# Optimization experiments

Hardware: AMD Instinct MI355X
Metric: run time of the kernel (lower is better)

The kernel has to match this reference:

```python
import jax, jax.numpy as jnp
import numpy as np

T, B, L, S = 2048, 64, 32, 256
NEG = -1e30  # effective -inf, safe under logaddexp


def setup_inputs() -> dict:
    key = jax.random.key(0)
    k1, k2, k3 = jax.random.split(key, 3)
    inputs = jax.random.normal(k1, (T, B, L), dtype=jnp.float32)
    targets = jax.random.randint(k2, (B, S), 0, L)
    input_lengths = jnp.full((B,), T, dtype=jnp.int32)
    target_lengths = jnp.full((B,), S, dtype=jnp.int32)
    # learned transition matrix (param of ASGLoss); small random for a non-trivial test
    transition = 0.1 * jax.random.normal(k3, (L, L), dtype=jnp.float32)
    return {"transition": transition, "inputs": inputs, "targets": targets,
            "input_lengths": input_lengths, "target_lengths": target_lengths}


def _fcc_scores(transition, inputs, input_lengths):
    # Fully-connected forward: alpha_t[i] = emit_t[i] + logsumexp_j(alpha_{t-1}[j] + trans[i,j])
    alpha0 = inputs[0]  # [B, L]

    def step(alpha, emit):
        new = emit + jax.nn.logsumexp(alpha[:, None, :] + transition[None, :, :], axis=2)
        return new, new

    _, rest = jax.lax.scan(step, alpha0, inputs[1:])
    alphas = jnp.concatenate([alpha0[None], rest], axis=0)  # [T, B, L]
    b = jnp.arange(inputs.shape[1])
    # causal DP: alpha at t = len-1 is exactly the score for that length
    return jax.nn.logsumexp(alphas[input_lengths - 1, b], axis=-1)  # [B]


def _fac_scores(transition, inputs, targets, input_lengths, target_lengths):
    # Force-aligned forward over target positions s:
    # alpha_t[s] = emit_t[tgt_s] + logaddexp(alpha_{t-1}[s] + trans[tgt_s,tgt_s],
    #                                        alpha_{t-1}[s-1] + trans[tgt_s,tgt_{s-1}])
    Tn, Bn, _ = inputs.shape
    Sn = targets.shape[1]
    # gathered emissions for target labels: [T, B, S]
    emit = jnp.take_along_axis(inputs, jnp.broadcast_to(targets[None], (Tn, Bn, Sn)), axis=2)
    self_tr = transition[targets, targets]                       # [B, S] stay score
    prev = jnp.concatenate([targets[:, :1], targets[:, :-1]], 1)
    move_tr = transition[targets, prev]                          # [B, S] move score (s=0 unused)

    alpha0 = jnp.where((jnp.arange(Sn) == 0)[None, :], emit[0], NEG)  # only s=0 at t=0

    def step(alpha, e):
        stay = alpha + self_tr
        moved = jnp.concatenate(
            [jnp.full_like(alpha[:, :1], NEG), alpha[:, :-1] + move_tr[:, 1:]], axis=1)
        new = e + jnp.logaddexp(stay, moved)
        return new, new

    _, rest = jax.lax.scan(step, alpha0, emit[1:])
    alphas = jnp.concatenate([alpha0[None], rest], axis=0)  # [T, B, S]
    b = jnp.arange(Bn)
    return alphas[input_lengths - 1, b, target_lengths - 1]  # [B]


def reference(transition, inputs, targets, input_lengths, target_lengths):
    # original clamps targets to input length; S <= T here so it's a no-op
    fcc = _fcc_scores(transition, inputs, input_lengths)
    fac = _fac_scores(transition, inputs, targets, input_lengths, target_lengths)
    result = fcc - fac  # [B]
    return result.mean()  # reduction='mean'
```

## Files before the change

kernel.cpp:

```cpp
#include <hip/hip_runtime.h>
#include <math.h>

static constexpr int TB = 64;
static constexpr int LL = 32;
static constexpr int SS = 256;
static constexpr int STRIDE_T = TB * LL;

static constexpr int NCH = 16;
static constexpr int NI  = NCH - 2;
static constexpr int NSCAN = 2 + 2 * NI;

static constexpr int OF_FCC  = 0;
static constexpr int OF_FACF = 992;
static constexpr int OF_FACB = 1312;
static constexpr int WSB     = 1632;
static constexpr int OF_DIFF = TB * WSB;

#define LN2F 0.69314718055994530942f
#define NEGF (-1e30f)
#define SBAR() __builtin_amdgcn_sched_barrier(0)

#define BARX() { asm volatile("s_waitcnt lgkmcnt(0)" ::: "memory"); \
                 __builtin_amdgcn_s_barrier(); \
                 asm volatile("" ::: "memory"); }

template<int CTL>
__device__ __forceinline__ float dpp_f(float x, float oldv) {
  return __int_as_float(__builtin_amdgcn_update_dpp(
      __float_as_int(oldv), __float_as_int(x), CTL, 0xF, 0xF, false));
}
template<int M>
__device__ __forceinline__ int rot_i(int x) {
  return __builtin_amdgcn_update_dpp(0, x, 0x120 + M, 0xF, 0xF, false);
}

typedef unsigned uint2v __attribute__((ext_vector_type(2)));
__device__ __forceinline__ float xsum16(float x) {
  uint2v r = __builtin_amdgcn_permlane16_swap(__float_as_uint(x), __float_as_uint(x), false, false);
  return __uint_as_float(r.x) + __uint_as_float(r.y);
}
__device__ __forceinline__ float xsum32(float x) {
  uint2v r = __builtin_amdgcn_permlane32_swap(__float_as_uint(x), __float_as_uint(x), false, false);
  return __uint_as_float(r.x) + __uint_as_float(r.y);
}
__device__ __forceinline__ float bperm(int addr, float src) {
  return __int_as_float(__builtin_amdgcn_ds_bpermute(addr, __float_as_int(src)));
}

template<int M>
struct Calib {
  __device__ static __forceinline__ void run(const float* trans, int lam, int i, float* Ec) {
    Ec[M] = __expf(trans[i * LL + rot_i<M>(lam)]);
    Calib<M + 1>::run(trans, lam, i, Ec);
  }
};
template<> struct Calib<16> {
  __device__ static __forceinline__ void run(const float*, int, int, float*) {}
};
template<int M>
struct CalibT {
  __device__ static __forceinline__ void run(const float* trans, int lam, int i, float* Ec) {
    Ec[M] = __expf(trans[rot_i<M>(lam) * LL + i]);
    CalibT<M + 1>::run(trans, lam, i, Ec);
  }
};
template<> struct CalibT<16> {
  __device__ static __forceinline__ void run(const float*, int, int, float*) {}
};

#define ROT_MUL(DST, SRC, COEF, ROT) \
  asm("v_mul_f32_dpp %0, %1, %2 row_ror:" #ROT " row_mask:0xf bank_mask:0xf" \
      : "=v"(DST) : "v"(SRC), "v"(COEF))
#define ROT_FMAC(ACC, SRC, COEF, ROT) \
  asm("v_fmac_f32_dpp %0, %1, %2 row_ror:" #ROT " row_mask:0xf bank_mask:0xf" \
      : "+v"(ACC) : "v"(SRC), "v"(COEF))

#define STEP16(EC) { \
  float a0 = EC[0] * A, a1, a2, a3, a4, a5, a6, a7; \
  ROT_MUL(a1, A, EC[1], 1); ROT_MUL(a2, A, EC[2], 2); ROT_MUL(a3, A, EC[3], 3); \
  ROT_MUL(a4, A, EC[4], 4); ROT_MUL(a5, A, EC[5], 5); ROT_MUL(a6, A, EC[6], 6); \
  ROT_MUL(a7, A, EC[7], 7); \
  ROT_FMAC(a0, A, EC[8], 8);   ROT_FMAC(a1, A, EC[9], 9); \
  ROT_FMAC(a2, A, EC[10], 10); ROT_FMAC(a3, A, EC[11], 11); \
  ROT_FMAC(a4, A, EC[12], 12); ROT_FMAC(a5, A, EC[13], 13); \
  ROT_FMAC(a6, A, EC[14], 14); ROT_FMAC(a7, A, EC[15], 15); \
  part = ((a0 + a1) + (a2 + a3)) + ((a4 + a5) + (a6 + a7)); }


#define FCC_RENORM() { \
  unsigned uu = (unsigned)__builtin_amdgcn_readfirstlane((int)__float_as_uint(A)); \
  int ex = (int)((uu >> 23) & 255) - 127; \
  A = ldexpf(A, -ex); Kt += ex; }

#define LDBLK(R, TBASE) { \
  _Pragma("unroll") for (int k = 0; k < 4; ++k) { \
    int tt = (TBASE) + 2 * k + rowoff; tt = tt > lenm1 ? lenm1 : tt; \
    R[k] = gpl[(size_t)tt * STRIDE_T]; } \
  SBAR(); }
#define LDBLKD(R, TBASE) { \
  _Pragma("unroll") for (int k = 0; k < 4; ++k) { \
    int tt = (TBASE) + 2 * k + rowoff; \
    tt = tt < 0 ? 0 : (tt > lenm1 ? lenm1 : tt); \
    R[k] = gpl[(size_t)tt * STRIDE_T]; } \
  SBAR(); }

#define FCC_BLOCK8(R) { \
  float eb[8]; \
  _Pragma("unroll") for (int k = 0; k < 4; ++k) { \
    float e_ = __expf(R[k]); \
    eb[2 * k]     = bperm(adE, e_); \
    eb[2 * k + 1] = bperm(adO, e_); } \
  { float part; STEP16(Ec1); A = eb[0] * xsum16(part); } \
  { float part; STEP16(Ec2); A = eb[1] * xsum32(part); } \
  { float part; STEP16(Ec1); A = eb[2] * xsum16(part); } \
  { float part; STEP16(Ec2); A = eb[3] * xsum32(part); } \
  { float part; STEP16(Ec1); A = eb[4] * xsum16(part); } \
  { float part; STEP16(Ec2); A = eb[5] * xsum32(part); } \
  { float part; STEP16(Ec1); A = eb[6] * xsum16(part); } \
  { float part; STEP16(Ec2); A = eb[7] * xsum32(part); } \
  FCC_RENORM(); }

#define FCC_BWDBLK8(R) { \
  float eb[8]; \
  _Pragma("unroll") for (int k = 0; k < 4; ++k) { \
    float e_ = __expf(R[k]); \
    eb[2 * k]     = bperm(adE, e_); \
    eb[2 * k + 1] = bperm(adO, e_); } \
  { A *= eb[7]; float part; STEP16(E1T); A = xsum16(part); } \
  { A *= eb[6]; float part; STEP16(E2T); A = xsum32(part); } \
  { A *= eb[5]; float part; STEP16(E1T); A = xsum16(part); } \
  { A *= eb[4]; float part; STEP16(E2T); A = xsum32(part); } \
  { A *= eb[3]; float part; STEP16(E1T); A = xsum16(part); } \
  { A *= eb[2]; float part; STEP16(E2T); A = xsum32(part); } \
  { A *= eb[1]; float part; STEP16(E1T); A = xsum16(part); } \
  { A *= eb[0]; float part; STEP16(E2T); A = xsum32(part); } \
  FCC_RENORM(); }


#define FAC_BOUNDARY_S() { \
  float maxA = fmaxf(fmaxf(A0, A1), fmaxf(A2, A3)); \
  if (maxA > 0.f) { \
    int ex = (int)((__float_as_uint(maxA) >> 23) & 255) - 127; \
    A0 = ldexpf(A0, -ex); A1 = ldexpf(A1, -ex); \
    A2 = ldexpf(A2, -ex); A3 = ldexpf(A3, -ex); \
    m += (float)ex; \
  } \
  float mp = dpp_f<0x138>(m, NEGF); m = (m == NEGF) ? mp : m; \
  mp = dpp_f<0x138>(m, NEGF);       m = (m == NEGF) ? mp : m; \
  mp = dpp_f<0x138>(m, NEGF); \
  float dlt = fminf(mp - m, 50.0f); \
  Sin = exp2f(dlt); }

#define FSTEPE(R) { \
  float c0 = Er[R].x * ST[0], c1 = Er[R].y * ST[1]; \
  float c2 = Er[R].z * ST[2], c3 = Er[R].w * ST[3]; \
  float v0 = Er[R].x * CM[0], v1 = Er[R].y * CM[1]; \
  float v2 = Er[R].z * CM[2], v3 = Er[R].w * CM[3]; \
  float ap = dpp_f<0x138>(A3, 0.f);  \
  float n0 = fmaf(v0 * Sin, ap, c0 * A0); \
  float n1 = fmaf(v1, A0, c1 * A1); \
  float n2 = fmaf(v2, A1, c2 * A2); \
  float n3 = fmaf(v3, A2, c3 * A3); \
  A0 = n0; A1 = n1; A2 = n2; A3 = n3; }

#define FRD16(PB, BASE) { \
  _Pragma("unroll") for (int r = 0; r < 16; ++r) Er[r] = sFE[PB][(BASE) + r][l]; }

#define FSTE8A() { FSTEPE(0); FSTEPE(1); FSTEPE(2); FSTEPE(3); \
                   FSTEPE(4); FSTEPE(5); FSTEPE(6); FSTEPE(7); }
#define FSTE8B() { FSTEPE(8); FSTEPE(9); FSTEPE(10); FSTEPE(11); \
                   FSTEPE(12); FSTEPE(13); FSTEPE(14); FSTEPE(15); }

#define FACF_CON32(PB) { \
  float4 Er[16]; \
  FRD16(PB, 0); \
  FSTE8A(); FAC_BOUNDARY_S(); \
  FSTE8B(); FAC_BOUNDARY_S(); \
  FRD16(PB, 16); \
  FSTE8A(); FAC_BOUNDARY_S(); \
  FSTE8B(); FAC_BOUNDARY_S(); }

#define FACF_TAIL32(PB, CNT) { \
  float4 Er[16]; \
  FRD16(PB, 0); \
  _Pragma("unroll") for (int r = 0; r < 16; ++r) { \
    if (r >= (CNT)) break; \
    FSTEPE(r); \
    if (r == 7) { FAC_BOUNDARY_S(); } } \
  if ((CNT) > 16) { \
    FAC_BOUNDARY_S(); \
    FRD16(PB, 16); \
    _Pragma("unroll") for (int r = 0; r < 16; ++r) { \
      if (r + 16 >= (CNT)) break; \
      FSTEPE(r); \
      if (r == 7) { FAC_BOUNDARY_S(); } } } }

#define FACB_BOUNDARY_S() { \
  float maxA = fmaxf(fmaxf(A0, A1), fmaxf(A2, A3)); \
  if (maxA > 0.f) { \
    int ex = (int)((__float_as_uint(maxA) >> 23) & 255) - 127; \
    A0 = ldexpf(A0, -ex); A1 = ldexpf(A1, -ex); \
    A2 = ldexpf(A2, -ex); A3 = ldexpf(A3, -ex); \
    m += (float)ex; \
  } \
  float mp = dpp_f<0x130>(m, NEGF); m = (m == NEGF) ? mp : m; \
  mp = dpp_f<0x130>(m, NEGF);       m = (m == NEGF) ? mp : m; \
  mp = dpp_f<0x130>(m, NEGF); \
  float dlt = fminf(mp - m, 50.0f); \
  Sb = exp2f(dlt); }

#define FBSTEPE(R) { \
  float c0 = Er[R].x * ST[0], c1 = Er[R].y * ST[1]; \
  float c2 = Er[R].z * ST[2], c3 = Er[R].w * ST[3]; \
  float w0 = Er[R].y * CM[0], w1 = Er[R].z * CM[1], w2 = Er[R].w * CM[2]; \
  float en3 = dpp_f<0x130>(Er[R].x, 0.f);  \
  float w3 = en3 * CM[3]; \
  float an = dpp_f<0x130>(A0, 0.f); \
  float n0 = fmaf(w0, A1, c0 * A0); \
  float n1 = fmaf(w1, A2, c1 * A1); \
  float n2 = fmaf(w2, A3, c2 * A2); \
  float n3 = fmaf(w3 * Sb, an, c3 * A3); \
  A0 = n0; A1 = n1; A2 = n2; A3 = n3; }

#define FBST8D() { FBSTEPE(15); FBSTEPE(14); FBSTEPE(13); FBSTEPE(12); \
                   FBSTEPE(11); FBSTEPE(10); FBSTEPE(9);  FBSTEPE(8); }
#define FBST8L() { FBSTEPE(7);  FBSTEPE(6);  FBSTEPE(5);  FBSTEPE(4); \
                   FBSTEPE(3);  FBSTEPE(2);  FBSTEPE(1);  FBSTEPE(0); }

#define FACB_CON32(PB) { \
  float4 Er[16]; \
  FRD16(PB, 16); \
  FBST8D(); FACB_BOUNDARY_S(); \
  FBST8L(); FACB_BOUNDARY_S(); \
  FRD16(PB, 0); \
  FBST8D(); FACB_BOUNDARY_S(); \
  FBST8L(); FACB_BOUNDARY_S(); }


#define FHLD32(Q, K) ({ \
  int tt_ = (isfwd ? (1 + 32 * (Q)) : (lenm1 - 32 * (Q) - 31)) + 2 * (K) + rowoff; \
  tt_ = tt_ < 0 ? 0 : (tt_ > lenm1 ? lenm1 : tt_); \
  gpl[(size_t)tt_ * STRIDE_T]; })

#define PRODE(PB, KK, RV) { \
  float e_ = __expf(RV); \
  float4 E0_, E1_; \
  E0_.x = bperm(adA[0], e_); E0_.y = bperm(adA[1], e_); \
  E0_.z = bperm(adA[2], e_); E0_.w = bperm(adA[3], e_); \
  E1_.x = bperm(adB[0], e_); E1_.y = bperm(adB[1], e_); \
  E1_.z = bperm(adB[2], e_); E1_.w = bperm(adB[3], e_); \
  sFE[PB][2 * (KK)][l]     = E0_; \
  sFE[PB][2 * (KK) + 1][l] = E1_; }


extern "C" __global__ __launch_bounds__(192, 1)
void asg_main(const float* __restrict__ trans, const float* __restrict__ inputs,
              const int* __restrict__ targets, const int* __restrict__ ilen,
              const int* __restrict__ tlen, float* __restrict__ ws) {
  const int tid = (int)threadIdx.x;
  const int w = tid >> 6;
  const int l = tid & 63;
  const int lam1 = l & 31;
  const int lam2 = (l & 15) | ((l >> 5) << 4);
  const int rowoff = l >> 5;
  const int bid = (int)blockIdx.x;

  __shared__ float4 sFE[2][32][64];

  if (bid < 2 * TB) {
    const int role = bid >> 6;
    const int b    = bid & 63;
    const int len = ilen[b];
    const int lenm1 = len - 1;
    const int Lsteps = lenm1;
    const int nbf = (Lsteps / 2) & ~31;
    const int nff = Lsteps - nbf;
    const bool isfwd = (role == 0);
    const int nsteps = isfwd ? nff : nbf;
    const int nph = (nsteps + 31) >> 5;
    const float* gpl = inputs + (size_t)b * LL + lam1;
    float* P = ws + (size_t)b * WSB;

    if (w == 0) {
      __builtin_amdgcn_s_setprio(1);
      int tg[4];
      #pragma unroll
      for (int q = 0; q < 4; ++q) tg[q] = targets[b * SS + 4 * l + q];
      float ST[4], CM[4];
      #pragma unroll
      for (int q = 0; q < 4; ++q) ST[q] = __expf(trans[tg[q] * LL + tg[q]]);

      if (isfwd) {
        CM[0] = (l == 0) ? 0.f : __expf(trans[tg[0] * LL + targets[b * SS + 4 * l - 1]]);
        #pragma unroll
        for (int q = 1; q < 4; ++q) CM[q] = __expf(trans[tg[q] * LL + tg[q - 1]]);

        float A0 = (l == 0) ? __expf(inputs[(size_t)b * LL + tg[0]]) : 0.f;
        float A1 = 0.f, A2 = 0.f, A3 = 0.f;
        float m  = (l == 0) ? 0.f : NEGF;
        float Sin;
        FAC_BOUNDARY_S();
        for (int p = 0; p < nph; p += 2) {
          BARX();
          { const int rem = nsteps - 32 * p;
            if (rem >= 32) { FACF_CON32(0); } else { FACF_TAIL32(0, rem); } }
          BARX();
          if (p + 1 < nph) {
            const int rem = nsteps - 32 * (p + 1);
            if (rem >= 32) { FACF_CON32(1); } else { FACF_TAIL32(1, rem); }
          }
        }
        P[OF_FACF + 4 * l + 0] = A0;
        P[OF_FACF + 4 * l + 1] = A1;
        P[OF_FACF + 4 * l + 2] = A2;
        P[OF_FACF + 4 * l + 3] = A3;
        P[OF_FACF + 256 + l]   = m;
      } else {
        CM[0] = __expf(trans[tg[1] * LL + tg[0]]);
        CM[1] = __expf(trans[tg[2] * LL + tg[1]]);
        CM[2] = __expf(trans[tg[3] * LL + tg[2]]);
        int tgn3 = (l < 63) ? targets[b * SS + 4 * l + 4] : 0;
        CM[3] = (l < 63) ? __expf(trans[tgn3 * LL + tg[3]]) : 0.f;

        const int tl = tlen[b];
        const int fs = tl - 1;
        float A0 = (4 * l + 0 == fs) ? 1.f : 0.f;
        float A1 = (4 * l + 1 == fs) ? 1.f : 0.f;
        float A2 = (4 * l + 2 == fs) ? 1.f : 0.f;
        float A3 = (4 * l + 3 == fs) ? 1.f : 0.f;
        float m  = (l == (fs >> 2)) ? 0.f : NEGF;
        float Sb;
        FACB_BOUNDARY_S();
        for (int p = 0; p < nph; p += 2) {
          BARX();
          FACB_CON32(0);
          BARX();
          if (p + 1 < nph) { FACB_CON32(1); }
        }
        P[OF_FACB + 4 * l + 0] = A0;
        P[OF_FACB + 4 * l + 1] = A1;
        P[OF_FACB + 4 * l + 2] = A2;
        P[OF_FACB + 4 * l + 3] = A3;
        P[OF_FACB + 256 + l]   = m;
      }
    } else {
      const int kh = 8 * (w - 1);
      int adA[4], adB[4];
      #pragma unroll
      for (int j = 0; j < 4; ++j) {
        int tg = targets[b * SS + 4 * l + j];
        adA[j] = tg * 4; adB[j] = adA[j] + 128;
      }
      float R1[8], R2[8], R3[8];
      #pragma unroll
      for (int k = 0; k < 8; ++k) R1[k] = FHLD32(0, kh + k);
      #pragma unroll
      for (int k = 0; k < 8; ++k) R2[k] = FHLD32(1, kh + k);
      #pragma unroll
      for (int k = 0; k < 8; ++k) R3[k] = FHLD32(2, kh + k);
      #pragma unroll
      for (int k = 0; k < 8; ++k) PRODE(0, kh + k, R1[k]);
      #pragma unroll
      for (int k = 0; k < 8; ++k) { R1[k] = R2[k]; R2[k] = R3[k]; R3[k] = FHLD32(3, kh + k); }

      for (int p = 0; p < nph; p += 2) {
        BARX();
        if (p + 1 < nph) {
          float N[8];
          #pragma unroll
          for (int k = 0; k < 8; ++k) N[k] = FHLD32(p + 4, kh + k);
          #pragma unroll
          for (int k = 0; k < 8; ++k) PRODE(1, kh + k, R1[k]);
          #pragma unroll
          for (int k = 0; k < 8; ++k) { R1[k] = R2[k]; R2[k] = R3[k]; R3[k] = N[k]; }
        }
        BARX();
        if (p + 2 < nph) {
          float N[8];
          #pragma unroll
          for (int k = 0; k < 8; ++k) N[k] = FHLD32(p + 5, kh + k);
          #pragma unroll
          for (int k = 0; k < 8; ++k) PRODE(0, kh + k, R1[k]);
          #pragma unroll
          for (int k = 0; k < 8; ++k) { R1[k] = R2[k]; R2[k] = R3[k]; R3[k] = N[k]; }
        }
      }
    }
    return;
  }

  const int cid = bid - 2 * TB;
  const int sid = 3 * cid + w;
  const int s = sid >> 6;
  const int b = sid & 63;
  const int len = ilen[b];
  const int lenm1 = len - 1;
  const int Lsteps = lenm1;
  int L = ((Lsteps / NCH) + 4) & ~7;
  if ((NCH - 1) * L > Lsteps) L = (Lsteps / NCH) & ~7;
  const int n0 = Lsteps - (NCH - 1) * L;

  bool isfwd; int t0 = 1, thi = lenm1, nsteps, outslot;
  if (s == 0)      { isfwd = true;  t0 = 1; nsteps = n0; outslot = 0; }
  else if (s == 1) { isfwd = false; thi = lenm1; nsteps = L; outslot = 1; }
  else {
    const int j = s >> 1;
    if ((s & 1) == 0) { isfwd = true;  t0 = n0 + (j - 1) * L + 1; nsteps = L; outslot = 2 * j; }
    else              { isfwd = false; thi = n0 + j * L;          nsteps = L; outslot = 2 * j + 1; }
  }
  const float* gpl = inputs + (size_t)b * LL + lam1;
  float* P = ws + (size_t)b * WSB + OF_FCC + outslot * 33;

  const int adE = lam2 * 4;
  const int adO = 128 + lam1 * 4;

  if (isfwd) {
    float Ec1[16], Ec2[16];
    Ec1[0] = __expf(trans[lam2 * LL + lam1]);
    Ec2[0] = __expf(trans[lam1 * LL + lam2]);
    Calib<1>::run(trans, lam1, lam2, Ec1);
    Calib<1>::run(trans, lam2, lam1, Ec2);
    float A = (s == 0) ? __expf(inputs[(size_t)b * LL + lam1]) : 1.f;
    int Kt = 0;
    int t = t0;
    const int tend = t0 + nsteps;
    float R0_[4], R1_[4], R2_[4];
    LDBLK(R0_, t); LDBLK(R1_, t + 8); LDBLK(R2_, t + 16);
    for (;;) {
      if (t + 8 > tend) break;
      FCC_BLOCK8(R0_); LDBLK(R0_, t + 24); t += 8;
      if (t + 8 > tend) break;
      FCC_BLOCK8(R1_); LDBLK(R1_, t + 24); t += 8;
      if (t + 8 > tend) break;
      FCC_BLOCK8(R2_); LDBLK(R2_, t + 24); t += 8;
    }
    if (t < tend) {
      float RT[4];
      LDBLK(RT, t);
      float eb[8];
      #pragma unroll
      for (int k = 0; k < 4; ++k) {
        float e_ = __expf(RT[k]);
        eb[2 * k]     = bperm(adE, e_);
        eb[2 * k + 1] = bperm(adO, e_);
      }
      #pragma unroll
      for (int q = 0; q < 8; ++q) {
        if (t + q >= tend) break;
        if ((q & 1) == 0) { float part; STEP16(Ec1); A = eb[q] * xsum16(part); }
        else              { float part; STEP16(Ec2); A = eb[q] * xsum32(part); }
      }
    }
    const int par = nsteps & 1;
    const int idx = par ? lam2 : lam1;
    const bool wr = par ? ((l & 16) == 0) : (l < 32);
    if (wr) P[idx] = A;
    if (l == 0) P[32] = (float)Kt;

  } else {
    float E1T[16], E2T[16];
    E1T[0] = __expf(trans[lam1 * LL + lam2]);
    E2T[0] = __expf(trans[lam2 * LL + lam1]);
    CalibT<1>::run(trans, lam1, lam2, E1T);
    CalibT<1>::run(trans, lam2, lam1, E2T);
    float A = 1.f;
    int Kt = 0;
    int th = thi;
    int rem = nsteps;
    float R0_[4], R1_[4], R2_[4];
    LDBLKD(R0_, th - 7); LDBLKD(R1_, th - 15); LDBLKD(R2_, th - 23);
    for (;;) {
      if (rem < 8) break;
      FCC_BWDBLK8(R0_); LDBLKD(R0_, th - 31); th -= 8; rem -= 8;
      if (rem < 8) break;
      FCC_BWDBLK8(R1_); LDBLKD(R1_, th - 31); th -= 8; rem -= 8;
      if (rem < 8) break;
      FCC_BWDBLK8(R2_); LDBLKD(R2_, th - 31); th -= 8; rem -= 8;
    }
    if (l < 32) P[lam1] = A;
    if (l == 0) P[32] = (float)Kt;
  }
}


extern "C" __global__ __launch_bounds__(64)
void asg_combineA(const float* __restrict__ ws, float* __restrict__ wdiff) {
  const int b = (int)blockIdx.x;
  const int l = (int)threadIdx.x;
  const float* P = ws + (size_t)b * WSB;

  float acc = 0.f;
  float Ksum = P[OF_FCC + 0 * 33 + 32];
  #pragma unroll
  for (int j = 0; j <= NI; ++j) {
    const int qs = (j == NI) ? 1 : (2 * j + 3);
    const int ps = (j == 0) ? 0 : (2 * j);
    float qv = (l < 32) ? P[OF_FCC + qs * 33 + l] : 0.f;
    float pv = (l < 32) ? P[OF_FCC + ps * 33 + l] : 0.f;
    float d = qv * pv;
    #pragma unroll
    for (int mm = 1; mm < 64; mm <<= 1) d += __shfl_xor(d, mm);
    acc += __logf(d);
    Ksum += P[OF_FCC + qs * 33 + 32];
  }
  #pragma unroll
  for (int j = 1; j <= NI; ++j) {
    float pv = (l < 32) ? P[OF_FCC + 2 * j * 33 + l] : 0.f;
    #pragma unroll
    for (int mm = 1; mm < 64; mm <<= 1) pv += __shfl_xor(pv, mm);
    acc -= __logf(pv);
  }
  float fcc = acc + Ksum * LN2F;

  float pa = P[OF_FACF + 4 * l + 0] * P[OF_FACB + 4 * l + 0]
           + P[OF_FACF + 4 * l + 1] * P[OF_FACB + 4 * l + 1]
           + P[OF_FACF + 4 * l + 2] * P[OF_FACB + 4 * l + 2]
           + P[OF_FACF + 4 * l + 3] * P[OF_FACB + 4 * l + 3];
  float sc = P[OF_FACF + 256 + l] + P[OF_FACB + 256 + l];
  float Ms = sc;
  #pragma unroll
  for (int mm = 1; mm < 64; mm <<= 1) Ms = fmaxf(Ms, __shfl_xor(Ms, mm));
  float pp = pa * exp2f(sc - Ms);
  #pragma unroll
  for (int mm = 1; mm < 64; mm <<= 1) pp += __shfl_xor(pp, mm);
  float fac = __logf(pp) + Ms * LN2F;

  if (l == 0) wdiff[b] = fcc - fac;
}

extern "C" __global__ __launch_bounds__(64)
void asg_combineB(const float* __restrict__ wdiff, float* __restrict__ out) {
  const int l = (int)threadIdx.x;
  float d = wdiff[l];
  #pragma unroll
  for (int mm = 1; mm < 64; mm <<= 1) d += __shfl_xor(d, mm);
  if (l == 0) out[0] = d * (1.0f / TB);
}


extern "C" void kernel_launch(void* const* d_in, const int* in_sizes, int n_in,
                              void* d_out, int out_size, void* d_ws, size_t ws_size,
                              hipStream_t stream) {
  const float* trans   = (const float*)d_in[0];
  const float* inputs  = (const float*)d_in[1];
  const int*   targets = (const int*)d_in[2];
  const int*   ilen    = (const int*)d_in[3];
  const int*   tlen    = (const int*)d_in[4];
  float* out = (float*)d_out;
  float* ws  = (float*)d_ws;

  asg_main<<<dim3(2 * TB + (NSCAN * TB) / 3), dim3(192), 0, stream>>>(
      trans, inputs, targets, ilen, tlen, ws);
  asg_combineA<<<dim3(TB), dim3(64), 0, stream>>>(ws, ws + OF_DIFF);
  asg_combineB<<<dim3(1), dim3(64), 0, stream>>>(ws + OF_DIFF, out);
}
```

Baseline: 77.37 us.

## Store raw exp-emissions in LDS and gather by target in consumer wave

The producer side shrinks from two waves that built per-lane float4 gathered emissions via bpermute to a single wave that writes exp(emissions) into a compact [32][32] LDS tile. The FAC scan wave now gathers the four target labels itself with indexed LDS reads, in groups of 8 steps. Blocks drop to 128 threads, and the scan blocks are remapped to 2 waves each with more blocks launched. The intent is to remove the bpermute work and the larger LDS footprint. The cost is scattered LDS reads on the latency-critical scan wave and a single producer wave that may fall behind.

```diff
diff --git a/kernel.cpp b/kernel.cpp
--- a/kernel.cpp
+++ b/kernel.cpp
@@ -151,50 +151,6 @@
   float dlt = fminf(mp - m, 50.0f); \
   Sin = exp2f(dlt); }
 
-#define FSTEPE(R) { \
-  float c0 = Er[R].x * ST[0], c1 = Er[R].y * ST[1]; \
-  float c2 = Er[R].z * ST[2], c3 = Er[R].w * ST[3]; \
-  float v0 = Er[R].x * CM[0], v1 = Er[R].y * CM[1]; \
-  float v2 = Er[R].z * CM[2], v3 = Er[R].w * CM[3]; \
-  float ap = dpp_f<0x138>(A3, 0.f);  \
-  float n0 = fmaf(v0 * Sin, ap, c0 * A0); \
-  float n1 = fmaf(v1, A0, c1 * A1); \
-  float n2 = fmaf(v2, A1, c2 * A2); \
-  float n3 = fmaf(v3, A2, c3 * A3); \
-  A0 = n0; A1 = n1; A2 = n2; A3 = n3; }
-
-#define FRD16(PB, BASE) { \
-  _Pragma("unroll") for (int r = 0; r < 16; ++r) Er[r] = sFE[PB][(BASE) + r][l]; }
-
-#define FSTE8A() { FSTEPE(0); FSTEPE(1); FSTEPE(2); FSTEPE(3); \
-                   FSTEPE(4); FSTEPE(5); FSTEPE(6); FSTEPE(7); }
-#define FSTE8B() { FSTEPE(8); FSTEPE(9); FSTEPE(10); FSTEPE(11); \
-                   FSTEPE(12); FSTEPE(13); FSTEPE(14); FSTEPE(15); }
-
-#define FACF_CON32(PB) { \
-  float4 Er[16]; \
-  FRD16(PB, 0); \
-  FSTE8A(); FAC_BOUNDARY_S(); \
-  FSTE8B(); FAC_BOUNDARY_S(); \
-  FRD16(PB, 16); \
-  FSTE8A(); FAC_BOUNDARY_S(); \
-  FSTE8B(); FAC_BOUNDARY_S(); }
-
-#define FACF_TAIL32(PB, CNT) { \
-  float4 Er[16]; \
-  FRD16(PB, 0); \
-  _Pragma("unroll") for (int r = 0; r < 16; ++r) { \
-    if (r >= (CNT)) break; \
-    FSTEPE(r); \
-    if (r == 7) { FAC_BOUNDARY_S(); } } \
-  if ((CNT) > 16) { \
-    FAC_BOUNDARY_S(); \
-    FRD16(PB, 16); \
-    _Pragma("unroll") for (int r = 0; r < 16; ++r) { \
-      if (r + 16 >= (CNT)) break; \
-      FSTEPE(r); \
-      if (r == 7) { FAC_BOUNDARY_S(); } } } }
-
 #define FACB_BOUNDARY_S() { \
   float maxA = fmaxf(fmaxf(A0, A1), fmaxf(A2, A3)); \
   if (maxA > 0.f) { \
@@ -209,11 +165,31 @@
   float dlt = fminf(mp - m, 50.0f); \
   Sb = exp2f(dlt); }
 
-#define FBSTEPE(R) { \
-  float c0 = Er[R].x * ST[0], c1 = Er[R].y * ST[1]; \
-  float c2 = Er[R].z * ST[2], c3 = Er[R].w * ST[3]; \
-  float w0 = Er[R].y * CM[0], w1 = Er[R].z * CM[1], w2 = Er[R].w * CM[2]; \
-  float en3 = dpp_f<0x130>(Er[R].x, 0.f);  \
+#define FRDGRP(PB, BASE) { \
+  _Pragma("unroll") for (int r = 0; r < 8; ++r) { \
+    e0[r] = sE[PB][(BASE) + r][tg[0]]; \
+    e1[r] = sE[PB][(BASE) + r][tg[1]]; \
+    e2[r] = sE[PB][(BASE) + r][tg[2]]; \
+    e3[r] = sE[PB][(BASE) + r][tg[3]]; } \
+  SBAR(); }
+
+#define FSTEPN(R) { \
+  float c0 = e0[R] * ST[0], c1 = e1[R] * ST[1]; \
+  float c2 = e2[R] * ST[2], c3 = e3[R] * ST[3]; \
+  float v0 = e0[R] * CM[0], v1 = e1[R] * CM[1]; \
+  float v2 = e2[R] * CM[2], v3 = e3[R] * CM[3]; \
+  float ap = dpp_f<0x138>(A3, 0.f);  \
+  float n0 = fmaf(v0 * Sin, ap, c0 * A0); \
+  float n1 = fmaf(v1, A0, c1 * A1); \
+  float n2 = fmaf(v2, A1, c2 * A2); \
+  float n3 = fmaf(v3, A2, c3 * A3); \
+  A0 = n0; A1 = n1; A2 = n2; A3 = n3; }
+
+#define FBSTEPN(R) { \
+  float c0 = e0[R] * ST[0], c1 = e1[R] * ST[1]; \
+  float c2 = e2[R] * ST[2], c3 = e3[R] * ST[3]; \
+  float w0 = e1[R] * CM[0], w1 = e2[R] * CM[1], w2 = e3[R] * CM[2]; \
+  float en3 = dpp_f<0x130>(e0[R], 0.f);  \
   float w3 = en3 * CM[3]; \
   float an = dpp_f<0x130>(A0, 0.f); \
   float n0 = fmaf(w0, A1, c0 * A0); \
@@ -222,38 +198,57 @@
   float n3 = fmaf(w3 * Sb, an, c3 * A3); \
   A0 = n0; A1 = n1; A2 = n2; A3 = n3; }
 
-#define FBST8D() { FBSTEPE(15); FBSTEPE(14); FBSTEPE(13); FBSTEPE(12); \
-                   FBSTEPE(11); FBSTEPE(10); FBSTEPE(9);  FBSTEPE(8); }
-#define FBST8L() { FBSTEPE(7);  FBSTEPE(6);  FBSTEPE(5);  FBSTEPE(4); \
-                   FBSTEPE(3);  FBSTEPE(2);  FBSTEPE(1);  FBSTEPE(0); }
-
-#define FACB_CON32(PB) { \
-  float4 Er[16]; \
-  FRD16(PB, 16); \
-  FBST8D(); FACB_BOUNDARY_S(); \
-  FBST8L(); FACB_BOUNDARY_S(); \
-  FRD16(PB, 0); \
-  FBST8D(); FACB_BOUNDARY_S(); \
-  FBST8L(); FACB_BOUNDARY_S(); }
-
-
-#define FHLD32(Q, K) ({ \
-  int tt_ = (isfwd ? (1 + 32 * (Q)) : (lenm1 - 32 * (Q) - 31)) + 2 * (K) + rowoff; \
-  tt_ = tt_ < 0 ? 0 : (tt_ > lenm1 ? lenm1 : tt_); \
-  gpl[(size_t)tt_ * STRIDE_T]; })
-
-#define PRODE(PB, KK, RV) { \
-  float e_ = __expf(RV); \
-  float4 E0_, E1_; \
-  E0_.x = bperm(adA[0], e_); E0_.y = bperm(adA[1], e_); \
-  E0_.z = bperm(adA[2], e_); E0_.w = bperm(adA[3], e_); \
-  E1_.x = bperm(adB[0], e_); E1_.y = bperm(adB[1], e_); \
-  E1_.z = bperm(adB[2], e_); E1_.w = bperm(adB[3], e_); \
-  sFE[PB][2 * (KK)][l]     = E0_; \
-  sFE[PB][2 * (KK) + 1][l] = E1_; }
-
-
-extern "C" __global__ __launch_bounds__(192, 1)
+#define FACF_CON32N(PB) { \
+  float e0[8], e1[8], e2[8], e3[8]; \
+  FRDGRP(PB, 0); \
+  _Pragma("unroll") for (int r = 0; r < 8; ++r) FSTEPN(r); \
+  FAC_BOUNDARY_S(); \
+  FRDGRP(PB, 8); \
+  _Pragma("unroll") for (int r = 0; r < 8; ++r) FSTEPN(r); \
+  FAC_BOUNDARY_S(); \
+  FRDGRP(PB, 16); \
+  _Pragma("unroll") for (int r = 0; r < 8; ++r) FSTEPN(r); \
+  FAC_BOUNDARY_S(); \
+  FRDGRP(PB, 24); \
+  _Pragma("unroll") for (int r = 0; r < 8; ++r) FSTEPN(r); \
+  FAC_BOUNDARY_S(); }
+
+#define FACF_TAIL32N(PB, CNT) { \
+  float e0[8], e1[8], e2[8], e3[8]; \
+  _Pragma("unroll") for (int g4 = 0; g4 < 4; ++g4) { \
+    if (8 * g4 >= (CNT)) break; \
+    FRDGRP(PB, 8 * g4); \
+    _Pragma("unroll") for (int r = 0; r < 8; ++r) { \
+      if (8 * g4 + r >= (CNT)) break; \
+      FSTEPN(r); } \
+    if (8 * g4 + 8 <= (CNT)) { FAC_BOUNDARY_S(); } } }
+
+#define FACB_CON32N(PB) { \
+  float e0[8], e1[8], e2[8], e3[8]; \
+  FRDGRP(PB, 24); \
+  _Pragma("unroll") for (int i = 0; i < 8; ++i) { const int r = 7 - i; FBSTEPN(r); } \
+  FACB_BOUNDARY_S(); \
+  FRDGRP(PB, 16); \
+  _Pragma("unroll") for (int i = 0; i < 8; ++i) { const int r = 7 - i; FBSTEPN(r); } \
+  FACB_BOUNDARY_S(); \
+  FRDGRP(PB, 8); \
+  _Pragma("unroll") for (int i = 0; i < 8; ++i) { const int r = 7 - i; FBSTEPN(r); } \
+  FACB_BOUNDARY_S(); \
+  FRDGRP(PB, 0); \
+  _Pragma("unroll") for (int i = 0; i < 8; ++i) { const int r = 7 - i; FBSTEPN(r); } \
+  FACB_BOUNDARY_S(); }
+
+#define PRODPH(PB, Q) { \
+  _Pragma("unroll") for (int k = 0; k < 16; ++k) { \
+    int tt = isfwd ? (1 + 32 * (Q) + 2 * k + rowoff) \
+                   : (lenm1 - 32 * (Q) - 31 + 2 * k + rowoff); \
+    tt = tt < 0 ? 0 : (tt > lenm1 ? lenm1 : tt); \
+    float e_ = __expf(gpl[(size_t)tt * STRIDE_T]); \
+    sE[PB][2 * k + rowoff][lam1] = e_; } \
+  SBAR(); }
+
+
+extern "C" __global__ __launch_bounds__(128, 1)
 void asg_main(const float* __restrict__ trans, const float* __restrict__ inputs,
               const int* __restrict__ targets, const int* __restrict__ ilen,
               const int* __restrict__ tlen, float* __restrict__ ws) {
@@ -265,7 +260,7 @@
   const int rowoff = l >> 5;
   const int bid = (int)blockIdx.x;
 
-  __shared__ float4 sFE[2][32][64];
+  __shared__ float sE[2][32][32];
 
   if (bid < 2 * TB) {
     const int role = bid >> 6;
@@ -303,11 +298,11 @@
         for (int p = 0; p < nph; p += 2) {
           BARX();
           { const int rem = nsteps - 32 * p;
-            if (rem >= 32) { FACF_CON32(0); } else { FACF_TAIL32(0, rem); } }
+            if (rem >= 32) { FACF_CON32N(0); } else { FACF_TAIL32N(0, rem); } }
           BARX();
           if (p + 1 < nph) {
             const int rem = nsteps - 32 * (p + 1);
-            if (rem >= 32) { FACF_CON32(1); } else { FACF_TAIL32(1, rem); }
+            if (rem >= 32) { FACF_CON32N(1); } else { FACF_TAIL32N(1, rem); }
           }
         }
         P[OF_FACF + 4 * l + 0] = A0;
@@ -333,9 +328,9 @@
         FACB_BOUNDARY_S();
         for (int p = 0; p < nph; p += 2) {
           BARX();
-          FACB_CON32(0);
+          FACB_CON32N(0);
           BARX();
-          if (p + 1 < nph) { FACB_CON32(1); }
+          if (p + 1 < nph) { FACB_CON32N(1); }
         }
         P[OF_FACB + 4 * l + 0] = A0;
         P[OF_FACB + 4 * l + 1] = A1;
@@ -344,53 +339,19 @@
         P[OF_FACB + 256 + l]   = m;
       }
     } else {
-      const int kh = 8 * (w - 1);
-      int adA[4], adB[4];
-      #pragma unroll
-      for (int j = 0; j < 4; ++j) {
-        int tg = targets[b * SS + 4 * l + j];
-        adA[j] = tg * 4; adB[j] = adA[j] + 128;
-      }
-      float R1[8], R2[8], R3[8];
-      #pragma unroll
-      for (int k = 0; k < 8; ++k) R1[k] = FHLD32(0, kh + k);
-      #pragma unroll
-      for (int k = 0; k < 8; ++k) R2[k] = FHLD32(1, kh + k);
-      #pragma unroll
-      for (int k = 0; k < 8; ++k) R3[k] = FHLD32(2, kh + k);
-      #pragma unroll
-      for (int k = 0; k < 8; ++k) PRODE(0, kh + k, R1[k]);
-      #pragma unroll
-      for (int k = 0; k < 8; ++k) { R1[k] = R2[k]; R2[k] = R3[k]; R3[k] = FHLD32(3, kh + k); }
-
+      PRODPH(0, 0);
       for (int p = 0; p < nph; p += 2) {
         BARX();
-        if (p + 1 < nph) {
-          float N[8];
-          #pragma unroll
-          for (int k = 0; k < 8; ++k) N[k] = FHLD32(p + 4, kh + k);
-          #pragma unroll
-          for (int k = 0; k < 8; ++k) PRODE(1, kh + k, R1[k]);
-          #pragma unroll
-          for (int k = 0; k < 8; ++k) { R1[k] = R2[k]; R2[k] = R3[k]; R3[k] = N[k]; }
-        }
+        if (p + 1 < nph) { PRODPH(1, p + 1); }
         BARX();
-        if (p + 2 < nph) {
-          float N[8];
-          #pragma unroll
-          for (int k = 0; k < 8; ++k) N[k] = FHLD32(p + 5, kh + k);
-          #pragma unroll
-          for (int k = 0; k < 8; ++k) PRODE(0, kh + k, R1[k]);
-          #pragma unroll
-          for (int k = 0; k < 8; ++k) { R1[k] = R2[k]; R2[k] = R3[k]; R3[k] = N[k]; }
-        }
+        if (p + 2 < nph) { PRODPH(0, p + 2); }
       }
     }
     return;
   }
 
   const int cid = bid - 2 * TB;
-  const int sid = 3 * cid + w;
+  const int sid = 2 * cid + w;
   const int s = sid >> 6;
   const int b = sid & 63;
   const int len = ilen[b];
@@ -549,7 +510,7 @@
   float* out = (float*)d_out;
   float* ws  = (float*)d_ws;
 
-  asg_main<<<dim3(2 * TB + (NSCAN * TB) / 3), dim3(192), 0, stream>>>(
+  asg_main<<<dim3(2 * TB + (NSCAN * TB) / 2), dim3(128), 0, stream>>>(
       trans, inputs, targets, ilen, tlen, ws);
   asg_combineA<<<dim3(TB), dim3(64), 0, stream>>>(ws, ws + OF_DIFF);
   asg_combineB<<<dim3(1), dim3(64), 0, stream>>>(ws + OF_DIFF, out);
```

After: 78.34 us. No clear change (+1.3%).
